# Performance work log

Hardware: AMD Instinct MI355X
Metric: run time of the kernel (lower is better)

## Reference

```python
import jax, jax.numpy as jnp
import numpy as np

N_HEAD, D_HEAD, EMBED = 16, 64, 1024
B, Q_LEN, MEM_LEN = 2, 1024, 1024
K_LEN = Q_LEN + MEM_LEN  # == r_len
LN_EPS = 1e-3  # keras LayerNormalization default


def rel_shift(x):
    # x: [B, H, q, r]  (Transformer-XL relative shift)
    b, h, q, r = x.shape
    x = jnp.pad(x, ((0, 0), (0, 0), (0, 0), (1, 0)))
    x = x.reshape(b, h, r + 1, q)[:, :, 1:, :]
    return x.reshape(b, h, q, r)


def setup_inputs() -> dict:
    key = jax.random.key(0)
    ks = jax.random.split(key, 12)
    s = 0.02
    w = jax.random.normal(ks[0], (B, Q_LEN, EMBED), jnp.float32)
    r = jax.random.normal(ks[1], (K_LEN, EMBED), jnp.float32)
    member = jax.random.normal(ks[2], (B, MEM_LEN, EMBED), jnp.float32)
    r_w_bias = jax.random.normal(ks[3], (N_HEAD, D_HEAD), jnp.float32) * s
    r_r_bias = jax.random.normal(ks[4], (N_HEAD, D_HEAD), jnp.float32) * s
    # causal mask over [q_len, k_len]: position i may attend to mem + keys <= mem_len+i
    qi = jnp.arange(Q_LEN)[:, None]
    kj = jnp.arange(K_LEN)[None, :]
    attn_mask = (kj > qi + MEM_LEN).astype(jnp.float32)
    Wq = jax.random.normal(ks[5], (EMBED, N_HEAD * D_HEAD), jnp.float32) * s
    Wk = jax.random.normal(ks[6], (EMBED, N_HEAD * D_HEAD), jnp.float32) * s
    Wv = jax.random.normal(ks[7], (EMBED, N_HEAD * D_HEAD), jnp.float32) * s
    Wr = jax.random.normal(ks[8], (EMBED, N_HEAD * D_HEAD), jnp.float32) * s
    Wo = jax.random.normal(ks[9], (N_HEAD * D_HEAD, EMBED), jnp.float32) * s
    ln_gamma = jnp.ones((EMBED,), jnp.float32)
    ln_beta = jnp.zeros((EMBED,), jnp.float32)
    return {"w": w, "r": r, "attn_mask": attn_mask, "r_w_bias": r_w_bias,
            "r_r_bias": r_r_bias, "member": member, "Wq": Wq, "Wk": Wk,
            "Wv": Wv, "Wr": Wr, "Wo": Wo, "ln_gamma": ln_gamma, "ln_beta": ln_beta}


def reference(w, r, attn_mask, r_w_bias, r_r_bias, member, Wq, Wk, Wv, Wr, Wo, ln_gamma, ln_beta):
    b, q_len, _ = w.shape
    cat = jnp.concatenate([member, w], axis=1)          # [B, klen, D]
    klen = cat.shape[1]
    q = (cat @ Wq)[:, -q_len:].reshape(b, q_len, N_HEAD, D_HEAD)
    k = (cat @ Wk).reshape(b, klen, N_HEAD, D_HEAD)
    v = (cat @ Wv).reshape(b, klen, N_HEAD, D_HEAD)
    rr = (r @ Wr).reshape(r.shape[0], N_HEAD, D_HEAD)    # [rlen, H, dh]
    rw_q = q + r_w_bias[None, None]                      # content bias
    rr_q = q + r_r_bias[None, None]                      # position bias
    AC = jnp.einsum('bqhd,bkhd->bhqk', rw_q, k)
    BD = jnp.einsum('bqhd,rhd->bhqr', rr_q, rr)
    BD = rel_shift(BD)
    attn = (AC + BD) / jnp.sqrt(jnp.float32(EMBED))      # note: sqrt(embed), as in source
    m = attn_mask[None, None]                            # [1,1,q,k]
    attn = attn * (1.0 - m) - 1e30 * m
    score = jax.nn.softmax(attn, axis=-1)
    out = jnp.einsum('bhqk,bkhd->bqhd', score, v).reshape(b, q_len, N_HEAD * D_HEAD)
    out = out @ Wo
    x = w + out
    mu = jnp.mean(x, axis=-1, keepdims=True)
    var = jnp.mean(jnp.square(x - mu), axis=-1, keepdims=True)
    return (x - mu) * jax.lax.rsqrt(var + LN_EPS) * ln_gamma + ln_beta
```

## Files before the change

### kernel.cpp

```cpp
#include <hip/hip_runtime.h>


typedef __bf16 bf16;
typedef __bf16 bf16x4 __attribute__((ext_vector_type(4)));
typedef __bf16 bf16x8 __attribute__((ext_vector_type(8)));
typedef float f32x4 __attribute__((ext_vector_type(4)));

#define MFMA16(a, b, c) __builtin_amdgcn_mfma_f32_16x16x32_bf16((a), (b), (c), 0, 0, 0)

constexpr int E = 1024;
constexpr int NH = 16;
constexpr int DH = 64;
constexpr int QL = 1024;
constexpr int ML = 1024;
constexpr int KLEN = 2048;

__device__ __forceinline__ void ldg2lds16(const bf16* g, bf16* l) {
    __builtin_amdgcn_global_load_lds(
        (const __attribute__((address_space(1))) unsigned int*)g,
        (__attribute__((address_space(3))) unsigned int*)l, 16, 0, 0);
}

__device__ __forceinline__ bf16x8 frag8(const bf16* t, int row, int ch) {
    return *(const bf16x8*)(t + row * 64 + ((ch ^ (row & 7)) << 3));
}

__global__ void pre_k(const float* __restrict__ Wq, const float* __restrict__ Wk,
                      const float* __restrict__ Wv, const float* __restrict__ Wr,
                      const float* __restrict__ Wo, const float* __restrict__ member,
                      const float* __restrict__ w, bf16* __restrict__ WqT,
                      bf16* __restrict__ WkT, bf16* __restrict__ WvT,
                      bf16* __restrict__ WrT, bf16* __restrict__ WoT,
                      bf16* __restrict__ cat) {
    const int id = blockIdx.x;
    const int tid = threadIdx.x;
    __shared__ float t[32][33];
    if (id < 5120) {
        const float* W; bf16* WT;
        switch (id >> 10) {
            case 0: W = Wq; WT = WqT; break;
            case 1: W = Wk; WT = WkT; break;
            case 2: W = Wv; WT = WvT; break;
            case 3: W = Wr; WT = WrT; break;
            default: W = Wo; WT = WoT; break;
        }
        int xy = id & 1023;
        int bx = (xy & 31) * 32, by = (xy >> 5) * 32;
        int x = tid & 31, y = tid >> 5;
        for (int yy = y; yy < 32; yy += 8)
            t[yy][x] = W[(by + yy) * E + bx + x];
        __syncthreads();
        for (int yy = y; yy < 32; yy += 8)
            WT[(bx + yy) * E + by + x] = (bf16)t[x][yy];
    } else {
        int row = id - 5120;
        int b = row >> 11, jj = row & 2047;
        const float* src = (jj < ML) ? member + ((size_t)(b * ML + jj)) * E
                                     : w + ((size_t)(b * QL + (jj - ML))) * E;
        float4 f = *(const float4*)(src + tid * 4);
        bf16x4 o;
        o[0] = (bf16)f.x; o[1] = (bf16)f.y; o[2] = (bf16)f.z; o[3] = (bf16)f.w;
        *(bf16x4*)(cat + (size_t)row * E + tid * 4) = o;
    }
}

__global__ __launch_bounds__(256) void proj_k(
    const bf16* __restrict__ cat, const float* __restrict__ r,
    const bf16* __restrict__ WqT, const bf16* __restrict__ WkT,
    const bf16* __restrict__ WvT, const bf16* __restrict__ WrT,
    const float* __restrict__ rwb, const float* __restrict__ rrb,
    bf16* __restrict__ Qw, bf16* __restrict__ Qr, bf16* __restrict__ Kh,
    bf16* __restrict__ Vt, bf16* __restrict__ RRh) {
    __shared__ __align__(16) bf16 As[128 * 64];
    __shared__ __align__(16) bf16 Bs[128 * 64];
    const int tid = threadIdx.x;
    const int wave = tid >> 6, lane = tid & 63, quad = lane >> 4, l16 = lane & 15;

    int id = blockIdx.x, zone, base;
    if (id < 128) { zone = 0; base = 0; }
    else if (id < 384) { zone = 1; base = 128; }
    else if (id < 640) { zone = 2; base = 384; }
    else { zone = 3; base = 640; }
    const int lid = id - base;
    const int bn = (lid & 7) * 128, bm = (lid >> 3) * 128;
    const bf16* Bt = (zone == 0) ? WqT : (zone == 1) ? WkT : (zone == 2) ? WvT : WrT;
    const int wm = (wave >> 1) * 64, wn = (wave & 1) * 64;

    f32x4 acc[4][4] = {};

    for (int kk = 0; kk < E; kk += 64) {
        if (zone == 3) {
            int srw = tid >> 3, cch = tid & 7;
            for (int c = 0; c < 4; ++c) {
                int row = c * 32 + srw;
                const float* ap = r + (size_t)(bm + row) * E + kk + cch * 8;
                float4 f0 = *(const float4*)ap;
                float4 f1 = *(const float4*)(ap + 4);
                bf16x8 v;
                v[0] = (bf16)f0.x; v[1] = (bf16)f0.y; v[2] = (bf16)f0.z; v[3] = (bf16)f0.w;
                v[4] = (bf16)f1.x; v[5] = (bf16)f1.y; v[6] = (bf16)f1.z; v[7] = (bf16)f1.w;
                *(bf16x8*)(As + row * 64 + ((cch ^ (row & 7)) << 3)) = v;
            }
        } else {
            for (int issue = 0; issue < 4; ++issue) {
                int q = (issue * 4 + wave) * 64 + lane;
                int row = q >> 3, cs = (q & 7) ^ ((q >> 3) & 7);
                int gm = bm + row;
                const bf16* ap;
                if (zone == 0) {
                    int b = gm >> 10;
                    ap = cat + ((size_t)(b * 2048 + 1024 + (gm & 1023))) * E;
                } else {
                    ap = cat + (size_t)gm * E;
                }
                ldg2lds16(ap + kk + cs * 8, As + (issue * 4 + wave) * 512);
            }
        }
        for (int issue = 0; issue < 4; ++issue) {
            int q = (issue * 4 + wave) * 64 + lane;
            int row = q >> 3, cs = (q & 7) ^ ((q >> 3) & 7);
            ldg2lds16(Bt + (size_t)(bn + row) * E + kk + cs * 8,
                      Bs + (issue * 4 + wave) * 512);
        }
        __syncthreads();
        for (int ks = 0; ks < 64; ks += 32) {
            bf16x8 af[4], bfr[4];
            for (int mt = 0; mt < 4; ++mt)
                af[mt] = frag8(As, wm + mt * 16 + l16, (ks >> 3) + quad);
            for (int nt = 0; nt < 4; ++nt)
                bfr[nt] = frag8(Bs, wn + nt * 16 + l16, (ks >> 3) + quad);
            for (int mt = 0; mt < 4; ++mt)
                for (int nt = 0; nt < 4; ++nt)
                    acc[mt][nt] = MFMA16(af[mt], bfr[nt], acc[mt][nt]);
        }
        __syncthreads();
    }

    if (zone == 2) {
        bf16* buf = ((wave < 2) ? As : Bs) + (wave & 1) * 4096;
        for (int mt = 0; mt < 4; ++mt)
            for (int nt = 0; nt < 4; ++nt)
                for (int rr = 0; rr < 4; ++rr) {
                    int lr = mt * 16 + quad * 4 + rr;
                    int lc = nt * 16 + l16;
                    buf[lr * 64 + (((lc >> 3) ^ (lr & 7)) << 3) + (lc & 7)] =
                        (bf16)acc[mt][nt][rr];
                }
        int h = (bn + wn) >> 6;
        int gmw = bm + wm;
        int b = gmw >> 11, jb = gmw & 2047;
        for (int dp = 0; dp < 8; ++dp) {
            int dl = dp * 8 + (lane >> 3);
            int jl = (lane & 7) * 8;
            bf16x8 tmp;
            for (int jj = 0; jj < 8; ++jj) {
                int rw = jl + jj;
                tmp[jj] = buf[rw * 64 + (((dl >> 3) ^ (rw & 7)) << 3) + (dl & 7)];
            }
            *(bf16x8*)(Vt + (((size_t)(b * NH + h) * DH + dl) * KLEN) + jb + jl) = tmp;
        }
        return;
    }

    for (int mt = 0; mt < 4; ++mt)
        for (int nt = 0; nt < 4; ++nt)
            for (int rr = 0; rr < 4; ++rr) {
                int row = bm + wm + mt * 16 + quad * 4 + rr;
                int col = bn + wn + nt * 16 + l16;
                float v = acc[mt][nt][rr];
                if (zone == 0) {
                    int b = row >> 10, i = row & 1023;
                    int h = col >> 6, d = col & 63;
                    size_t o = (((size_t)(b * NH + h) * QL) + i) * DH + d;
                    Qw[o] = (bf16)((v + rwb[col]) * 0.03125f);
                    Qr[o] = (bf16)((v + rrb[col]) * 0.03125f);
                } else if (zone == 1) {
                    int b = row >> 11, j = row & 2047;
                    int h = col >> 6, d = col & 63;
                    Kh[(((size_t)(b * NH + h) * KLEN) + j) * DH + d] = (bf16)v;
                } else {
                    int h = col >> 6, d = col & 63;
                    RRh[(((size_t)h * KLEN) + row) * DH + d] = (bf16)v;
                }
            }
}

__global__ __launch_bounds__(512, 4) void attn_k(
    const bf16* __restrict__ Qw, const bf16* __restrict__ Qr,
    const bf16* __restrict__ Kh, const bf16* __restrict__ Vt,
    const bf16* __restrict__ RRh, bf16* __restrict__ AttO) {
    __shared__ __align__(16) bf16 Ks[2][64 * 64];
    __shared__ __align__(16) bf16 Vs[2][64 * 64];
    __shared__ __align__(16) bf16 RRing[3][64 * 64];
    __shared__ __align__(16) bf16 UB[2][4][16 * 88];

    const int tid = threadIdx.x;
    const int wave = tid >> 6, lane = tid & 63, quad = lane >> 4, l16 = lane & 15;
    const int id = blockIdx.x;
    const int b = id >> 8, h = (id >> 4) & 15;
    const int qt = (id < 256) ? (id & 15) : (15 - (id & 15));
    const int i0 = qt * 64;
    const bool isS = wave < 4;
    const int sw = isS ? wave : wave - 4;

    const bf16* Qwb = Qw + ((size_t)(b * NH + h) * QL) * DH;
    const bf16* Qrb = Qr + ((size_t)(b * NH + h) * QL) * DH;
    const bf16* Kb = Kh + ((size_t)(b * NH + h) * KLEN) * DH;
    const bf16* Vb = Vt + ((size_t)(b * NH + h) * DH) * KLEN;
    const bf16* Rb = RRh + ((size_t)h * KLEN) * DH;

    bf16x8 qw0, qw1, qr0, qr1;
    if (isS) {
        int i = i0 + sw * 16 + l16;
        qw0 = *(const bf16x8*)(Qwb + (size_t)i * DH + quad * 8);
        qw1 = *(const bf16x8*)(Qwb + (size_t)i * DH + 32 + quad * 8);
        qr0 = *(const bf16x8*)(Qrb + (size_t)i * DH + quad * 8);
        qr1 = *(const bf16x8*)(Qrb + (size_t)i * DH + 32 + quad * 8);
    }

    float lpart[4] = {0.f, 0.f, 0.f, 0.f};
    f32x4 oacc[4] = {};

    const int ntiles = qt + 17;
    const int cbase = 15 - qt;
    const int ptbase = 3 - sw;

    auto stageK = [&](int t) {
        int q = wave * 64 + lane;
        int row = q >> 3, cs = (q & 7) ^ (row & 7);
        ldg2lds16(Kb + (size_t)(t * 64 + row) * DH + cs * 8,
                  Ks[t & 1] + wave * 512);
    };
    auto stageV = [&](int t) {
        int q = wave * 64 + lane;
        int row = q >> 3, cs = (q & 7) ^ (row & 7);
        ldg2lds16(Vb + (size_t)row * KLEN + t * 64 + cs * 8,
                  Vs[t & 1] + wave * 512);
    };
    auto stageRR = [&](int c) {
        int q = wave * 64 + lane;
        int row = q >> 3, cs = (q & 7) ^ (row & 7);
        int pr = c * 64 + row;
        pr = pr > KLEN - 1 ? KLEN - 1 : pr;
        ldg2lds16(Rb + (size_t)pr * DH + cs * 8, RRing[c % 3] + wave * 512);
    };

    stageK(0);
    stageRR(cbase);
    stageRR(cbase + 1);
    __syncthreads();

    for (int p = 0; p <= ntiles; ++p) {
        if (p + 1 < ntiles) {
            stageK(p + 1);
            stageRR(cbase + p + 2);
        }
        if (p < ntiles) stageV(p);

        if (isS) {
            __builtin_amdgcn_s_setprio(1);
            if (p < ntiles) {
                const bf16* Kt = Ks[p & 1];
                const bf16* Rlo = RRing[(cbase + p) % 3];
                const bf16* Rhi = RRing[(cbase + p + 1) % 3];

                f32x4 bacc[5];
                for (int pi = 0; pi < 5; ++pi) {
                    int pt = ptbase + pi;
                    const bf16* Rsrc = (pt < 4) ? Rlo : Rhi;
                    int rrow = (pt & 3) * 16 + l16;
                    f32x4 a = {};
                    a = MFMA16(qr0, frag8(Rsrc, rrow, quad), a);
                    a = MFMA16(qr1, frag8(Rsrc, rrow, 4 + quad), a);
                    bacc[pi] = a;
                }

                f32x4 sacc[4];
                for (int nt = 0; nt < 4; ++nt) {
                    f32x4 a = {};
                    a = MFMA16(qw0, frag8(Kt, nt * 16 + l16, quad), a);
                    a = MFMA16(qw1, frag8(Kt, nt * 16 + l16, 4 + quad), a);
                    sacc[nt] = a;
                }

                float sv[4][4];
                const bool lastt = (p == ntiles - 1);
                for (int rr = 0; rr < 4; ++rr) {
                    const int lr = quad * 4 + rr;
                    const int srcl = quad * 16 + ((l16 - lr - 1) & 15);
                    float g[5];
                    for (int pi = 0; pi < 5; ++pi) g[pi] = __shfl(bacc[pi][rr], srcl);
                    const bool hi = (l16 > lr);
                    for (int nt = 0; nt < 4; ++nt) {
                        float bdv = hi ? g[nt + 1] : g[nt];
                        float pv = __expf(sacc[nt][rr] + bdv);
                        if (lastt) {
                            int i = i0 + sw * 16 + lr;
                            int j = p * 64 + nt * 16 + l16;
                            if (j > i + ML) pv = 0.f;
                        }
                        sv[nt][rr] = pv;
                        lpart[rr] += pv;
                    }
                }

                bf16* UBd = UB[p & 1][sw];
                for (int nt = 0; nt < 4; ++nt)
                    for (int rr = 0; rr < 4; ++rr)
                        UBd[(quad * 4 + rr) * 88 + nt * 16 + l16] = (bf16)sv[nt][rr];
            } else {
                float* lp = (float*)(&UB[ntiles & 1][sw][0]);
                for (int rr = 0; rr < 4; ++rr) {
                    float v = lpart[rr];
                    v += __shfl_xor(v, 1);
                    v += __shfl_xor(v, 2);
                    v += __shfl_xor(v, 4);
                    v += __shfl_xor(v, 8);
                    lp[lane * 4 + rr] = 1.f / v;
                }
            }
            __builtin_amdgcn_s_setprio(0);
        } else if (p >= 1) {
            const bf16* Vl = Vs[(p - 1) & 1];
            const bf16* UBs = UB[(p - 1) & 1][sw];
            for (int c = 0; c < 2; ++c) {
                bf16x8 pa = *(const bf16x8*)(&UBs[l16 * 88 + c * 32 + quad * 8]);
                for (int nt = 0; nt < 4; ++nt) {
                    bf16x8 vb = frag8(Vl, nt * 16 + l16, c * 4 + quad);
                    oacc[nt] = MFMA16(pa, vb, oacc[nt]);
                }
            }
        }
        __syncthreads();
    }

    if (!isS) {
        const float* lp = (const float*)(&UB[ntiles & 1][sw][0]);
        for (int nt = 0; nt < 4; ++nt)
            for (int rr = 0; rr < 4; ++rr) {
                int i = i0 + sw * 16 + quad * 4 + rr;
                int d = nt * 16 + l16;
                AttO[((size_t)(b * QL + i)) * E + h * DH + d] =
                    (bf16)(oacc[nt][rr] * lp[lane * 4 + rr]);
            }
    }
}

__global__ __launch_bounds__(256) void gemm_o(
    const bf16* __restrict__ A, const bf16* __restrict__ Bt,
    float* __restrict__ Xp, float* __restrict__ Xp3) {
    __shared__ __align__(16) bf16 As[128 * 64];
    __shared__ __align__(16) bf16 Bs[128 * 64];
    const int tid = threadIdx.x;
    const int wave = tid >> 6, lane = tid & 63, quad = lane >> 4, l16 = lane & 15;
    const int bm = blockIdx.y * 128, bn = blockIdx.x * 128;
    const int kbase = blockIdx.z * 256;
    const int wm = (wave >> 1) * 64, wn = (wave & 1) * 64;

    f32x4 acc[4][4] = {};

    for (int s = 0; s < 4; ++s) {
        const int kk = kbase + s * 64;
        for (int issue = 0; issue < 4; ++issue) {
            int q = (issue * 4 + wave) * 64 + lane;
            int row = q >> 3, cs = (q & 7) ^ ((q >> 3) & 7);
            ldg2lds16(A + (size_t)(bm + row) * E + kk + cs * 8,
                      As + (issue * 4 + wave) * 512);
            ldg2lds16(Bt + (size_t)(bn + row) * E + kk + cs * 8,
                      Bs + (issue * 4 + wave) * 512);
        }
        __syncthreads();
        for (int ks = 0; ks < 64; ks += 32) {
            bf16x8 af[4], bfr[4];
            for (int mt = 0; mt < 4; ++mt)
                af[mt] = frag8(As, wm + mt * 16 + l16, (ks >> 3) + quad);
            for (int nt = 0; nt < 4; ++nt)
                bfr[nt] = frag8(Bs, wn + nt * 16 + l16, (ks >> 3) + quad);
            for (int mt = 0; mt < 4; ++mt)
                for (int nt = 0; nt < 4; ++nt)
                    acc[mt][nt] = MFMA16(af[mt], bfr[nt], acc[mt][nt]);
        }
        __syncthreads();
    }

    float* Xz = (blockIdx.z == 3) ? Xp3
                                  : Xp + (size_t)blockIdx.z * 2048 * 1024;
    for (int mt = 0; mt < 4; ++mt)
        for (int nt = 0; nt < 4; ++nt)
            for (int rr = 0; rr < 4; ++rr) {
                int row = bm + wm + mt * 16 + quad * 4 + rr;
                int col = bn + wn + nt * 16 + l16;
                Xz[(size_t)row * E + col] = acc[mt][nt][rr];
            }
}

__global__ __launch_bounds__(256) void ln_k(const float* __restrict__ Xp,
                                            const float* __restrict__ Xp3,
                                            const float* __restrict__ resid,
                                            const float* __restrict__ gamma,
                                            const float* __restrict__ beta,
                                            float* __restrict__ out) {
    const int row = blockIdx.x;
    const int tid = threadIdx.x;
    const float* x0 = Xp + (size_t)row * E;
    const float* x1 = Xp + (size_t)2048 * 1024 + (size_t)row * E;
    const float* x2 = Xp + (size_t)2 * 2048 * 1024 + (size_t)row * E;
    const float* x3 = Xp3 + (size_t)row * E;
    const float* xr = resid + (size_t)row * E;
    float xv[4], s = 0.f, q = 0.f;
    for (int c = 0; c < 4; ++c) {
        int col = c * 256 + tid;
        float v = x0[col] + x1[col] + x2[col] + x3[col] + xr[col];
        xv[c] = v;
        s += v;
        q += v * v;
    }
    for (int off = 32; off > 0; off >>= 1) {
        s += __shfl_down(s, off);
        q += __shfl_down(q, off);
    }
    __shared__ float rs[4], rq[4];
    int wave = tid >> 6, lane = tid & 63;
    if (lane == 0) { rs[wave] = s; rq[wave] = q; }
    __syncthreads();
    float S = rs[0] + rs[1] + rs[2] + rs[3];
    float Q = rq[0] + rq[1] + rq[2] + rq[3];
    float mean = S * (1.f / E);
    float var = fmaxf(Q * (1.f / E) - mean * mean, 0.f);
    float rstd = rsqrtf(var + 1e-3f);
    for (int c = 0; c < 4; ++c) {
        int col = c * 256 + tid;
        out[(size_t)row * E + col] =
            (xv[c] - mean) * rstd * gamma[col] + beta[col];
    }
}

extern "C" void kernel_launch(void* const* d_in, const int* in_sizes, int n_in,
                              void* d_out, int out_size, void* d_ws,
                              size_t ws_size, hipStream_t stream) {
    (void)in_sizes; (void)n_in; (void)out_size; (void)ws_size;
    const float* w = (const float*)d_in[0];
    const float* r = (const float*)d_in[1];
    const float* rwb = (const float*)d_in[3];
    const float* rrb = (const float*)d_in[4];
    const float* member = (const float*)d_in[5];
    const float* Wq = (const float*)d_in[6];
    const float* Wk = (const float*)d_in[7];
    const float* Wv = (const float*)d_in[8];
    const float* Wr = (const float*)d_in[9];
    const float* Wo = (const float*)d_in[10];
    const float* gamma = (const float*)d_in[11];
    const float* beta = (const float*)d_in[12];
    float* out = (float*)d_out;

    char* ws = (char*)d_ws;
    const size_t MB = 1024 * 1024;
    bf16* WqT = (bf16*)(ws + 0 * MB);
    bf16* WkT = (bf16*)(ws + 2 * MB);
    bf16* WvT = (bf16*)(ws + 4 * MB);
    bf16* WrT = (bf16*)(ws + 6 * MB);
    bf16* WoT = (bf16*)(ws + 8 * MB);
    bf16* cat = (bf16*)(ws + 10 * MB);
    bf16* AttO = (bf16*)(ws + 14 * MB);
    bf16* Qw = (bf16*)(ws + 18 * MB);
    bf16* Qr = (bf16*)(ws + 22 * MB);
    float* Xp = (float*)(ws + 18 * MB);
    bf16* Kh = (bf16*)(ws + 26 * MB);
    bf16* Vt = (bf16*)(ws + 34 * MB);
    bf16* RRh = (bf16*)(ws + 42 * MB);
    float* Xp3 = (float*)(ws + 0 * MB);

    pre_k<<<9216, 256, 0, stream>>>(Wq, Wk, Wv, Wr, Wo, member, w, WqT, WkT,
                                    WvT, WrT, WoT, cat);

    proj_k<<<768, 256, 0, stream>>>(cat, r, WqT, WkT, WvT, WrT, rwb, rrb, Qw,
                                    Qr, Kh, Vt, RRh);

    attn_k<<<512, 512, 0, stream>>>(Qw, Qr, Kh, Vt, RRh, AttO);

    gemm_o<<<dim3(8, 16, 4), 256, 0, stream>>>(AttO, WoT, Xp, Xp3);
    ln_k<<<2048, 256, 0, stream>>>(Xp, Xp3, w, gamma, beta, out);
}
```

Baseline: 247.9 us.

## Software-pipeline score MFMAs one tile ahead and remap blocks across XCDs

Splits the score-wave work into an MFMA phase and an exp/softmax VALU phase, issuing the next tile's MFMAs right after the current tile's VALU work so matrix and vector units can overlap. K and RR staging now run two tiles ahead to feed this. Block IDs are also remapped so each XCD gets a fixed set of (batch, head) pairs in both q-tile directions, aiming for better L2 reuse of K/V/RR and balanced causal work. The risks are higher register pressure from keeping bacc/sacc live across iterations, and K being staged two ahead into a two-slot buffer, which only stays correct if barrier placement protects it.

Result: slower. 276.8 us (+11.7%).

```diff
diff --git a/kernel.cpp b/kernel.cpp
--- a/kernel.cpp
+++ b/kernel.cpp
@@ -197,8 +197,14 @@
     const int tid = threadIdx.x;
     const int wave = tid >> 6, lane = tid & 63, quad = lane >> 4, l16 = lane & 15;
     const int id = blockIdx.x;
-    const int b = id >> 8, h = (id >> 4) & 15;
-    const int qt = (id < 256) ? (id & 15) : (15 - (id & 15));
+    const int xcd = id & 7;
+    const int v6 = id >> 3;
+    const int dir = (v6 >> 5) & 1;
+    const int hs = (v6 >> 4) & 1;
+    const int q4 = v6 & 15;
+    const int qt = dir ? (15 - q4) : q4;
+    const int combo = xcd * 4 + hs * 2 + dir;
+    const int b = combo >> 4, h = combo & 15;
     const int i0 = qt * 64;
     const bool isS = wave < 4;
     const int sw = isS ? wave : wave - 4;
@@ -220,6 +226,7 @@
 
     float lpart[4] = {0.f, 0.f, 0.f, 0.f};
     f32x4 oacc[4] = {};
+    f32x4 bacc[5], sacc[4];
 
     const int ntiles = qt + 17;
     const int cbase = 15 - qt;
@@ -245,69 +252,74 @@
         ldg2lds16(Rb + (size_t)pr * DH + cs * 8, RRing[c % 3] + wave * 512);
     };
 
+    auto mfma_tile = [&](int t) {
+        const bf16* Kt = Ks[t & 1];
+        const bf16* Rlo = RRing[(cbase + t) % 3];
+        const bf16* Rhi = RRing[(cbase + t + 1) % 3];
+        for (int pi = 0; pi < 5; ++pi) {
+            int pt = ptbase + pi;
+            const bf16* Rsrc = (pt < 4) ? Rlo : Rhi;
+            int rrow = (pt & 3) * 16 + l16;
+            f32x4 a = {};
+            a = MFMA16(qr0, frag8(Rsrc, rrow, quad), a);
+            a = MFMA16(qr1, frag8(Rsrc, rrow, 4 + quad), a);
+            bacc[pi] = a;
+        }
+        for (int nt = 0; nt < 4; ++nt) {
+            f32x4 a = {};
+            a = MFMA16(qw0, frag8(Kt, nt * 16 + l16, quad), a);
+            a = MFMA16(qw1, frag8(Kt, nt * 16 + l16, 4 + quad), a);
+            sacc[nt] = a;
+        }
+    };
+
+    auto valu_tile = [&](int p) {
+        float sv[4][4];
+        const bool lastt = (p == ntiles - 1);
+        for (int rr = 0; rr < 4; ++rr) {
+            const int lr = quad * 4 + rr;
+            const int srcl = quad * 16 + ((l16 - lr - 1) & 15);
+            float g[5];
+            for (int pi = 0; pi < 5; ++pi) g[pi] = __shfl(bacc[pi][rr], srcl);
+            const bool hi = (l16 > lr);
+            for (int nt = 0; nt < 4; ++nt) {
+                float bdv = hi ? g[nt + 1] : g[nt];
+                float pv = __expf(sacc[nt][rr] + bdv);
+                if (lastt) {
+                    int i = i0 + sw * 16 + lr;
+                    int j = p * 64 + nt * 16 + l16;
+                    if (j > i + ML) pv = 0.f;
+                }
+                sv[nt][rr] = pv;
+                lpart[rr] += pv;
+            }
+        }
+        bf16* UBd = UB[p & 1][sw];
+        for (int nt = 0; nt < 4; ++nt)
+            for (int rr = 0; rr < 4; ++rr)
+                UBd[(quad * 4 + rr) * 88 + nt * 16 + l16] = (bf16)sv[nt][rr];
+    };
+
     stageK(0);
+    stageK(1);
     stageRR(cbase);
     stageRR(cbase + 1);
+    stageRR(cbase + 2);
     __syncthreads();
+    if (isS) mfma_tile(0);
 
     for (int p = 0; p <= ntiles; ++p) {
-        if (p + 1 < ntiles) {
-            stageK(p + 1);
-            stageRR(cbase + p + 2);
+        if (p + 3 <= ntiles) {
+            stageK(p + 2);
+            stageRR(cbase + p + 3);
         }
         if (p < ntiles) stageV(p);
 
         if (isS) {
             __builtin_amdgcn_s_setprio(1);
             if (p < ntiles) {
-                const bf16* Kt = Ks[p & 1];
-                const bf16* Rlo = RRing[(cbase + p) % 3];
-                const bf16* Rhi = RRing[(cbase + p + 1) % 3];
-
-                f32x4 bacc[5];
-                for (int pi = 0; pi < 5; ++pi) {
-                    int pt = ptbase + pi;
-                    const bf16* Rsrc = (pt < 4) ? Rlo : Rhi;
-                    int rrow = (pt & 3) * 16 + l16;
-                    f32x4 a = {};
-                    a = MFMA16(qr0, frag8(Rsrc, rrow, quad), a);
-                    a = MFMA16(qr1, frag8(Rsrc, rrow, 4 + quad), a);
-                    bacc[pi] = a;
-                }
-
-                f32x4 sacc[4];
-                for (int nt = 0; nt < 4; ++nt) {
-                    f32x4 a = {};
-                    a = MFMA16(qw0, frag8(Kt, nt * 16 + l16, quad), a);
-                    a = MFMA16(qw1, frag8(Kt, nt * 16 + l16, 4 + quad), a);
-                    sacc[nt] = a;
-                }
-
-                float sv[4][4];
-                const bool lastt = (p == ntiles - 1);
-                for (int rr = 0; rr < 4; ++rr) {
-                    const int lr = quad * 4 + rr;
-                    const int srcl = quad * 16 + ((l16 - lr - 1) & 15);
-                    float g[5];
-                    for (int pi = 0; pi < 5; ++pi) g[pi] = __shfl(bacc[pi][rr], srcl);
-                    const bool hi = (l16 > lr);
-                    for (int nt = 0; nt < 4; ++nt) {
-                        float bdv = hi ? g[nt + 1] : g[nt];
-                        float pv = __expf(sacc[nt][rr] + bdv);
-                        if (lastt) {
-                            int i = i0 + sw * 16 + lr;
-                            int j = p * 64 + nt * 16 + l16;
-                            if (j > i + ML) pv = 0.f;
-                        }
-                        sv[nt][rr] = pv;
-                        lpart[rr] += pv;
-                    }
-                }
-
-                bf16* UBd = UB[p & 1][sw];
-                for (int nt = 0; nt < 4; ++nt)
-                    for (int rr = 0; rr < 4; ++rr)
-                        UBd[(quad * 4 + rr) * 88 + nt * 16 + l16] = (bf16)sv[nt][rr];
+                valu_tile(p);
+                if (p + 1 < ntiles) mfma_tile(p + 1);
             } else {
                 float* lp = (float*)(&UB[ntiles & 1][sw][0]);
                 for (int rr = 0; rr < 4; ++rr) {
```
